# Performance work log

Hardware: AMD Instinct MI355X
Metric: run time of the kernel (lower is better)

Reference implementation:

```python
import jax, jax.numpy as jnp
import numpy as np

DIM = 1024
N_HEADS = 16
HEAD_DIM = DIM // N_HEADS
SCALE = HEAD_DIM ** 0.5


def setup_inputs() -> dict:
    key = jax.random.key(0)
    k_x, k_wqkv, k_bqkv, k_wp, k_bp = jax.random.split(key, 5)
    B, S = 4, 2048
    x = jax.random.normal(k_x, (B, S, DIM), dtype=jnp.float32)
    # Linear params stored input-major: y = x @ W + b
    std_qkv = 1.0 / np.sqrt(DIM)
    W_qkv = jax.random.uniform(k_wqkv, (DIM, 3 * DIM), jnp.float32, -std_qkv, std_qkv)
    b_qkv = jax.random.uniform(k_bqkv, (3 * DIM,), jnp.float32, -std_qkv, std_qkv)
    W_proj = jax.random.uniform(k_wp, (DIM, DIM), jnp.float32, -std_qkv, std_qkv)
    b_proj = jax.random.uniform(k_bp, (DIM,), jnp.float32, -std_qkv, std_qkv)
    return {"x": x, "W_qkv": W_qkv, "b_qkv": b_qkv, "W_proj": W_proj, "b_proj": b_proj}


def reference(x, W_qkv, b_qkv, W_proj, b_proj):
    B, S, D = x.shape
    qkv = x @ W_qkv + b_qkv                       # [B,S,3D]
    Q, K, V = jnp.split(qkv, 3, axis=-1)          # each [B,S,D]
    def heads(t):                                 # [B,S,D] -> [B,H,S,hd]
        return t.reshape(B, S, N_HEADS, HEAD_DIM).transpose(0, 2, 1, 3)
    Q, K, V = heads(Q), heads(K), heads(V)
    scores = jnp.einsum('bhqd,bhkd->bhqk', Q, K) / SCALE   # [B,H,S,S]
    attn = jax.nn.softmax(scores, axis=-1)
    out = jnp.einsum('bhqk,bhkd->bhqd', attn, V)           # [B,H,S,hd]
    out = out.transpose(0, 2, 1, 3).reshape(B, S, D)
    return out @ W_proj + b_proj
```

## Files before the change

kernel.cpp:

```cpp
#include <hip/hip_runtime.h>
#include <hip/hip_bf16.h>

typedef __attribute__((ext_vector_type(8))) __bf16 bf16x8;
typedef __attribute__((ext_vector_type(4))) float f32x4;
typedef __attribute__((ext_vector_type(16))) float f32x16;
typedef __attribute__((ext_vector_type(4))) unsigned int u32x4;

#define DIM 1024
#define NHEADS 16
#define HDIM 64
#define BATCH 4
#define SEQ 2048
#define ROWS (BATCH * SEQ)
#define SCL 0.18033688011112042f

__device__ inline unsigned short f2bf(float f) {
    __hip_bfloat16 h = __float2bfloat16(f);
    return *reinterpret_cast<unsigned short*>(&h);
}

__device__ inline unsigned int packbf2(float a, float b) {
    unsigned short ua = __builtin_bit_cast(unsigned short, (__bf16)a);
    unsigned short ub = __builtin_bit_cast(unsigned short, (__bf16)b);
    return (unsigned int)ua | ((unsigned int)ub << 16);
}

typedef const __attribute__((address_space(1))) unsigned int* gas_ptr;
typedef __attribute__((address_space(3))) unsigned int* las_ptr;
__device__ inline void gload16(const void* g, void* l) {
    __builtin_amdgcn_global_load_lds((gas_ptr)g, (las_ptr)l, 16, 0, 0);
}

__global__ __launch_bounds__(256) void cast_f32_bf16(const float* __restrict__ in,
                                                     unsigned short* __restrict__ out,
                                                     int n4) {
    int i = blockIdx.x * 256 + threadIdx.x;
    if (i < n4) {
        float4 v = ((const float4*)in)[i];
        ushort4 o;
        o.x = f2bf(v.x); o.y = f2bf(v.y); o.z = f2bf(v.z); o.w = f2bf(v.w);
        ((ushort4*)out)[i] = o;
    }
}

__global__ __launch_bounds__(256) void transpose_cast(const float* __restrict__ in,
                                                      unsigned short* __restrict__ out,
                                                      int R, int C, int srows, float scl) {
    __shared__ float tile[32][33];
    int c0 = blockIdx.x * 32, r0 = blockIdx.y * 32;
    int tx = threadIdx.x & 31, ty = threadIdx.x >> 5;
#pragma unroll
    for (int i = 0; i < 32; i += 8) {
        int r = r0 + ty + i, c = c0 + tx;
        tile[ty + i][tx] = in[(size_t)r * C + c];
    }
    __syncthreads();
#pragma unroll
    for (int i = 0; i < 32; i += 8) {
        int orow = c0 + ty + i, oc = r0 + tx;
        float v = tile[tx][ty + i];
        if (orow < srows) v *= scl;
        out[(size_t)orow * R + oc] = f2bf(v);
    }
}

__global__ __launch_bounds__(256) void gemm_bt_bias(const unsigned short* __restrict__ A,
                                                    const unsigned short* __restrict__ Bt,
                                                    const float* __restrict__ bias,
                                                    unsigned short* __restrict__ Cq,
                                                    unsigned short* __restrict__ Ckv,
                                                    float* __restrict__ Cf,
                                                    int M, int N, int K, int qcols) {
    __shared__ unsigned short As[2][128 * 32];
    __shared__ unsigned short Bs[2][128 * 32];
    const int tid = threadIdx.x;
    const int lane = tid & 63, wave = tid >> 6;
    const int wm = (wave >> 1) * 64, wn = (wave & 1) * 64;
    const int rowA = blockIdx.y * 128, rowB = blockIdx.x * 128;
    const int fr = lane & 15, fo = (lane >> 4) * 8;

    f32x4 acc[4][4] = {};

    for (int k0 = 0; k0 < K; k0 += 64) {
#pragma unroll
        for (int kc = 0; kc < 2; kc++) {
#pragma unroll
            for (int c = 0; c < 2; c++) {
                int o = c * 4096 + tid * 16;
                int r = o >> 6, cb = o & 63;
                int ldsb = c * 4096 + wave * 1024;
                gload16((const char*)A + ((size_t)(rowA + r) * K + k0 + kc * 32) * 2 + cb,
                        (char*)As[kc] + ldsb);
                gload16((const char*)Bt + ((size_t)(rowB + r) * K + k0 + kc * 32) * 2 + cb,
                        (char*)Bs[kc] + ldsb);
            }
        }
        __syncthreads();
#pragma unroll
        for (int kc = 0; kc < 2; kc++) {
            bf16x8 af[4], bfr[4];
#pragma unroll
            for (int i = 0; i < 4; i++) {
                af[i]  = *(const bf16x8*)(As[kc] + (wm + i * 16 + fr) * 32 + fo);
                bfr[i] = *(const bf16x8*)(Bs[kc] + (wn + i * 16 + fr) * 32 + fo);
            }
#pragma unroll
            for (int mi = 0; mi < 4; mi++)
#pragma unroll
                for (int ni = 0; ni < 4; ni++)
                    acc[mi][ni] = __builtin_amdgcn_mfma_f32_16x16x32_bf16(af[mi], bfr[ni],
                                                                          acc[mi][ni], 0, 0, 0);
        }
        __syncthreads();
    }

    const int cn = lane & 15, cm = (lane >> 4) * 4;
    for (int ni = 0; ni < 4; ni++) {
        int gn = rowB + wn + ni * 16 + cn;
        float bv = bias[gn];
        if (gn < qcols) bv *= SCL;
        for (int mi = 0; mi < 4; mi++) {
#pragma unroll
            for (int r = 0; r < 4; r++) {
                int gm = rowA + wm + mi * 16 + cm + r;
                float v = acc[mi][ni][r] + bv;
                if (Cf) Cf[(size_t)gm * N + gn] = v;
                else if (gn < 1024) Cq[(size_t)gm * 1024 + gn] = f2bf(v);
                else Ckv[(size_t)gm * 2048 + (gn - 1024)] = f2bf(v);
            }
        }
    }
}

__global__ __launch_bounds__(256) void pack_kv(const unsigned short* __restrict__ KVb,
                                               unsigned short* __restrict__ Kp,
                                               unsigned short* __restrict__ Vp) {
    __shared__ unsigned short Kt[64][72];
    __shared__ unsigned short Vt[64][68];
    const int tid = threadIdx.x;
    const int s0 = blockIdx.x * 64;
    const int by = blockIdx.y;
    const int b = by >> 4, h = by & 15;
    const size_t rowbase = ((size_t)(b * SEQ + s0)) * 2048 + h * 64;
    const int c = (tid & 7) * 8, rr = tid >> 3;
#pragma unroll
    for (int p = 0; p < 2; p++) {
        int row = p * 32 + rr;
        const unsigned short* src = KVb + rowbase + (size_t)row * 2048;
        uint4 kv = *(const uint4*)(src + c);
        uint4 vv = *(const uint4*)(src + 1024 + c);
        *(uint2*)&Kt[row][c]     = make_uint2(kv.x, kv.y);
        *(uint2*)&Kt[row][c + 4] = make_uint2(kv.z, kv.w);
        *(uint2*)&Vt[row][c]     = make_uint2(vv.x, vv.y);
        *(uint2*)&Vt[row][c + 4] = make_uint2(vv.z, vv.w);
    }
    __syncthreads();
#pragma unroll
    for (int half = 0; half < 2; half++) {
        int f = half * 256 + tid;
        int ktl = f >> 8, ks = (f >> 6) & 3, ln = f & 63;
        int mm = ln & 31, hh = ln >> 5;
        uint4 d = *(const uint4*)&Kt[ktl * 32 + mm][ks * 16 + hh * 8];
        *(uint4*)(Kp + (((size_t)by * 64 + (s0 >> 5) + ktl) * 4 + ks) * 512 + ln * 8) = d;
    }
#pragma unroll
    for (int half = 0; half < 2; half++) {
        int f = half * 256 + tid;
        int ksl = f >> 7, dt = (f >> 6) & 1, ln = f & 63;
        int mm = ln & 31, hh = ln >> 5;
        unsigned short tmp[8];
#pragma unroll
        for (int j = 0; j < 8; j++)
            tmp[j] = Vt[ksl * 16 + (j & 3) + 8 * (j >> 2) + 4 * hh][dt * 32 + mm];
        *(uint4*)(Vp + (((size_t)by * 128 + (s0 >> 4) + ksl) * 2 + dt) * 512 + ln * 8) =
            *(uint4*)tmp;
    }
}

__global__ __launch_bounds__(256, 2) void attn_kernel(const unsigned short* __restrict__ Qb,
                                                      const unsigned short* __restrict__ Kp,
                                                      const unsigned short* __restrict__ Vp,
                                                      unsigned short* __restrict__ attnb) {
    const int tid = threadIdx.x;
    const int lane = tid & 63, wave = tid >> 6;
    const int m31 = lane & 31, h = lane >> 5;
    const int by = blockIdx.y;
    const int b = by >> 4;
    const int bS = b * SEQ, hcol = (by & 15) * HDIM;
    const int q0 = blockIdx.x * 256 + wave * 64;

    bf16x8 qf[2][4];
#pragma unroll
    for (int qt = 0; qt < 2; qt++)
#pragma unroll
        for (int ks = 0; ks < 4; ks++)
            qf[qt][ks] = *(const bf16x8*)(Qb + (size_t)(bS + q0 + qt * 32 + m31) * 1024 +
                                          hcol + ks * 16 + h * 8);

    f32x16 oacc[2][2] = {};
    float psum[2] = {0.f, 0.f};

    const unsigned short* kbase = Kp + (size_t)by * 64 * 2048 + lane * 8;
    const unsigned short* vbase = Vp + (size_t)by * 128 * 1024 + lane * 8;

#pragma unroll 2
    for (int ku = 0; ku < SEQ / 32; ku++) {
        const unsigned short* kp = kbase + (size_t)ku * 2048;
        bf16x8 kf[4];
#pragma unroll
        for (int ks = 0; ks < 4; ks++) kf[ks] = *(const bf16x8*)(kp + ks * 512);
        bf16x8 vf[2][2];
#pragma unroll
        for (int ks = 0; ks < 2; ks++) {
            const unsigned short* vp = vbase + ((size_t)ku * 2 + ks) * 1024;
            vf[ks][0] = *(const bf16x8*)(vp);
            vf[ks][1] = *(const bf16x8*)(vp + 512);
        }
#pragma unroll
        for (int qt = 0; qt < 2; qt++) {
            f32x16 cfrag = {};
#pragma unroll
            for (int ks = 0; ks < 4; ks++)
                cfrag = __builtin_amdgcn_mfma_f32_32x32x16_bf16(kf[ks], qf[qt][ks],
                                                                cfrag, 0, 0, 0);
            unsigned int pk[8];
            float ls = 0.f;
#pragma unroll
            for (int p = 0; p < 8; p++) {
                float e0 = __builtin_amdgcn_exp2f(cfrag[2 * p]);
                float e1 = __builtin_amdgcn_exp2f(cfrag[2 * p + 1]);
                ls += e0 + e1;
                pk[p] = packbf2(e0, e1);
            }
            psum[qt] += ls;
            u32x4 lo = {pk[0], pk[1], pk[2], pk[3]};
            u32x4 hi = {pk[4], pk[5], pk[6], pk[7]};
            bf16x8 pa0 = __builtin_bit_cast(bf16x8, lo);
            bf16x8 pa1 = __builtin_bit_cast(bf16x8, hi);
            oacc[qt][0] = __builtin_amdgcn_mfma_f32_32x32x16_bf16(pa0, vf[0][0], oacc[qt][0], 0, 0, 0);
            oacc[qt][1] = __builtin_amdgcn_mfma_f32_32x32x16_bf16(pa0, vf[0][1], oacc[qt][1], 0, 0, 0);
            oacc[qt][0] = __builtin_amdgcn_mfma_f32_32x32x16_bf16(pa1, vf[1][0], oacc[qt][0], 0, 0, 0);
            oacc[qt][1] = __builtin_amdgcn_mfma_f32_32x32x16_bf16(pa1, vf[1][1], oacc[qt][1], 0, 0, 0);
        }
    }

#pragma unroll
    for (int qt = 0; qt < 2; qt++) {
        float lt = psum[qt] + __shfl_xor(psum[qt], 32, 64);
        float rl = 1.f / lt;
#pragma unroll
        for (int r = 0; r < 16; r++) {
            int row = (r & 3) + 8 * (r >> 2) + 4 * h;
            float rlr = __shfl(rl, row, 64);
            size_t orow = (size_t)(bS + q0 + qt * 32 + row) * 1024 + hcol;
            attnb[orow + m31]      = f2bf(oacc[qt][0][r] * rlr);
            attnb[orow + 32 + m31] = f2bf(oacc[qt][1][r] * rlr);
        }
    }
}

extern "C" void kernel_launch(void* const* d_in, const int* in_sizes, int n_in,
                              void* d_out, int out_size, void* d_ws, size_t ws_size,
                              hipStream_t stream) {
    const float* x      = (const float*)d_in[0];
    const float* W_qkv  = (const float*)d_in[1];
    const float* b_qkv  = (const float*)d_in[2];
    const float* W_proj = (const float*)d_in[3];
    const float* b_proj = (const float*)d_in[4];
    float* out = (float*)d_out;

    char* ws = (char*)d_ws;
    unsigned short* x_bf   = (unsigned short*)(ws);
    unsigned short* WqkvT  = (unsigned short*)(ws + 16777216);
    unsigned short* Qb     = (unsigned short*)(ws + 23068672);
    unsigned short* KVb    = (unsigned short*)(ws + 39845888);
    unsigned short* Kp     = (unsigned short*)(ws);
    unsigned short* Vp     = (unsigned short*)(ws + 73400320);
    unsigned short* attnb  = (unsigned short*)(ws + 39845888);
    unsigned short* WprojT = (unsigned short*)(ws + 90177536);

    cast_f32_bf16<<<(ROWS * DIM / 4 + 255) / 256, 256, 0, stream>>>(x, x_bf, ROWS * DIM / 4);
    transpose_cast<<<dim3(3 * DIM / 32, DIM / 32), 256, 0, stream>>>(W_qkv, WqkvT, DIM, 3 * DIM, DIM, SCL);
    transpose_cast<<<dim3(DIM / 32, DIM / 32), 256, 0, stream>>>(W_proj, WprojT, DIM, DIM, 0, 1.f);

    gemm_bt_bias<<<dim3(3 * DIM / 128, ROWS / 128), 256, 0, stream>>>(
        x_bf, WqkvT, b_qkv, Qb, KVb, nullptr, ROWS, 3 * DIM, DIM, DIM);

    pack_kv<<<dim3(SEQ / 64, BATCH * NHEADS), 256, 0, stream>>>(KVb, Kp, Vp);

    attn_kernel<<<dim3(SEQ / 256, BATCH * NHEADS), 256, 0, stream>>>(Qb, Kp, Vp, attnb);

    gemm_bt_bias<<<dim3(DIM / 128, ROWS / 128), 256, 0, stream>>>(
        attnb, WprojT, b_proj, nullptr, nullptr, out, ROWS, DIM, DIM, 0);
}
```

Baseline: 298.5 us.

## Split attention key range across two waves and reduce partials in shared memory

```diff
diff --git a/kernel.cpp b/kernel.cpp
--- a/kernel.cpp
+++ b/kernel.cpp
@@ -177,17 +177,23 @@
     }
 }
 
-__global__ __launch_bounds__(256, 2) void attn_kernel(const unsigned short* __restrict__ Qb,
+__global__ __launch_bounds__(128, 4) void attn_kernel(const unsigned short* __restrict__ Qb,
                                                       const unsigned short* __restrict__ Kp,
                                                       const unsigned short* __restrict__ Vp,
                                                       unsigned short* __restrict__ attnb) {
+    __shared__ float Po[16 * 256];
+    __shared__ float Pl[128];
     const int tid = threadIdx.x;
     const int lane = tid & 63, wave = tid >> 6;
     const int m31 = lane & 31, h = lane >> 5;
-    const int by = blockIdx.y;
+
+    const int gid = blockIdx.x;
+    const int slot = gid >> 3;
+    const int by = (gid & 7) * 8 + (slot >> 5);
+    const int qt5 = slot & 31;
     const int b = by >> 4;
     const int bS = b * SEQ, hcol = (by & 15) * HDIM;
-    const int q0 = blockIdx.x * 256 + wave * 64;
+    const int q0 = qt5 * 64;
 
     bf16x8 qf[2][4];
 #pragma unroll
@@ -203,8 +209,10 @@
     const unsigned short* kbase = Kp + (size_t)by * 64 * 2048 + lane * 8;
     const unsigned short* vbase = Vp + (size_t)by * 128 * 1024 + lane * 8;
 
+    const int ku0 = wave * 32;
 #pragma unroll 2
-    for (int ku = 0; ku < SEQ / 32; ku++) {
+    for (int ki = 0; ki < 32; ki++) {
+        int ku = ku0 + ki;
         const unsigned short* kp = kbase + (size_t)ku * 2048;
         bf16x8 kf[4];
 #pragma unroll
@@ -244,17 +252,46 @@
         }
     }
 
-#pragma unroll
-    for (int qt = 0; qt < 2; qt++) {
-        float lt = psum[qt] + __shfl_xor(psum[qt], 32, 64);
-        float rl = 1.f / lt;
-#pragma unroll
-        for (int r = 0; r < 16; r++) {
-            int row = (r & 3) + 8 * (r >> 2) + 4 * h;
-            float rlr = __shfl(rl, row, 64);
-            size_t orow = (size_t)(bS + q0 + qt * 32 + row) * 1024 + hcol;
-            attnb[orow + m31]      = f2bf(oacc[qt][0][r] * rlr);
-            attnb[orow + 32 + m31] = f2bf(oacc[qt][1][r] * rlr);
+    if (wave == 1) {
+#pragma unroll
+        for (int qt = 0; qt < 2; qt++)
+#pragma unroll
+            for (int dt = 0; dt < 2; dt++)
+#pragma unroll
+                for (int c = 0; c < 4; c++) {
+                    f32x4 v = {oacc[qt][dt][c * 4 + 0], oacc[qt][dt][c * 4 + 1],
+                               oacc[qt][dt][c * 4 + 2], oacc[qt][dt][c * 4 + 3]};
+                    *(f32x4*)&Po[(qt * 8 + dt * 4 + c) * 256 + lane * 4] = v;
+                }
+        *(float2*)&Pl[lane * 2] = make_float2(psum[0], psum[1]);
+    }
+    __syncthreads();
+    if (wave == 0) {
+#pragma unroll
+        for (int qt = 0; qt < 2; qt++)
+#pragma unroll
+            for (int dt = 0; dt < 2; dt++)
+#pragma unroll
+                for (int c = 0; c < 4; c++) {
+                    f32x4 v = *(const f32x4*)&Po[(qt * 8 + dt * 4 + c) * 256 + lane * 4];
+#pragma unroll
+                    for (int j = 0; j < 4; j++) oacc[qt][dt][c * 4 + j] += v[j];
+                }
+        float2 pl = *(const float2*)&Pl[lane * 2];
+        psum[0] += pl.x; psum[1] += pl.y;
+
+#pragma unroll
+        for (int qt = 0; qt < 2; qt++) {
+            float lt = psum[qt] + __shfl_xor(psum[qt], 32, 64);
+            float rl = 1.f / lt;
+#pragma unroll
+            for (int r = 0; r < 16; r++) {
+                int row = (r & 3) + 8 * (r >> 2) + 4 * h;
+                float rlr = __shfl(rl, row, 64);
+                size_t orow = (size_t)(bS + q0 + qt * 32 + row) * 1024 + hcol;
+                attnb[orow + m31]      = f2bf(oacc[qt][0][r] * rlr);
+                attnb[orow + 32 + m31] = f2bf(oacc[qt][1][r] * rlr);
+            }
         }
     }
 }
@@ -288,7 +325,7 @@
 
     pack_kv<<<dim3(SEQ / 64, BATCH * NHEADS), 256, 0, stream>>>(KVb, Kp, Vp);
 
-    attn_kernel<<<dim3(SEQ / 256, BATCH * NHEADS), 256, 0, stream>>>(Qb, Kp, Vp, attnb);
+    attn_kernel<<<dim3(64 * (SEQ / 64)), 128, 0, stream>>>(Qb, Kp, Vp, attnb);
 
     gemm_bt_bias<<<dim3(DIM / 128, ROWS / 128), 256, 0, stream>>>(
         attnb, WprojT, b_proj, nullptr, nullptr, out, ROWS, DIM, DIM, 0);
```

After: 689.8 us. 2.31x slower.
